# Performance work log

Measured on AMD Instinct MI355X. Metric: run time of the kernel, lower is better.

## Reference

```python
import jax, jax.numpy as jnp
import numpy as np

G1 = 3.0  # cfg.TRAIN.IoU_Gamma1
G2 = 1.0  # cfg.TRAIN.IoU_Gamma2


def setup_inputs() -> dict:
    key = jax.random.key(0)
    ks = jax.random.split(key, 5)
    B, N = 16, 2048
    cls = 0.3 * jax.random.normal(ks[0], (B, N, 2), jnp.float32)
    label_cls = jax.random.randint(ks[1], (B, N), 0, 2).astype(jnp.int32)
    label_loc = jax.random.normal(ks[2], (B, 4, N), jnp.float32)
    pred_bboxes = jax.random.uniform(ks[3], (B, 4, N), jnp.float32)
    label_target = jax.random.uniform(ks[4], (B, 4), jnp.float32)
    dataset_id = jnp.zeros((B,), jnp.int32)
    return dict(cls=cls, label_cls=label_cls, label_loc=label_loc,
                pred_bboxes=pred_bboxes, label_target=label_target,
                dataset_id=dataset_id)


def _iou(boxes, target):
    # boxes [B,4,N] (x1,y1,x2,y2); target [B,4]
    x1, y1, x2, y2 = boxes[:, 0], boxes[:, 1], boxes[:, 2], boxes[:, 3]
    tx1, ty1, tx2, ty2 = (target[:, 0:1], target[:, 1:2],
                          target[:, 2:3], target[:, 3:4])
    ww = jnp.clip(jnp.minimum(tx2, x2) - jnp.maximum(tx1, x1), 0.0)
    hh = jnp.clip(jnp.minimum(ty2, y2) - jnp.maximum(ty1, y1), 0.0)
    area = (x2 - x1) * (y2 - y1)
    ta = (tx2 - tx1) * (ty2 - ty1)
    inter = ww * hh
    return inter / (area + ta - inter)  # [B,N]


def _forward(cls, label_loc, pred_bboxes, label_target, label_cls, dataset_id):
    prob = jnp.exp(cls[..., 1])                      # [B,N]
    pos = label_cls > 0                              # [B,N]
    iou = _iou(pred_bboxes, label_target)            # [B,N]
    # centerness distance to target center
    cx = label_loc[:, 0] + label_target[:, 0:1]      # [B,N]
    cy = label_loc[:, 1] + label_target[:, 1:2]
    tcx = (label_target[:, 0] + label_target[:, 2]) * 0.5
    tcy = (label_target[:, 1] + label_target[:, 3]) * 0.5
    d = jnp.sqrt((cx - tcx[:, None]) ** 2 + (cy - tcy[:, None]) ** 2)  # [B,N]
    # pair (p,q): both positive, d[q]-d[p] >= 1.0 (== nested sorted-loop selection)
    pair = (pos[:, :, None] & pos[:, None, :]
            & ((d[:, None, :] - d[:, :, None]) >= 1.0))               # [B,N,N]
    m = pair.astype(prob.dtype)
    cnt = m.sum((1, 2))                                               # [B]
    # guard exponent with the mask to avoid inf*0 on dead pairs
    e1 = jnp.where(pair, -G1 * (prob[:, :, None] - prob[:, None, :]), 0.0)
    iou_sg = jax.lax.stop_gradient(iou)
    e2 = jnp.where(pair, -G2 * (iou[:, :, None] - iou_sg[:, None, :]), 0.0)
    denom = jnp.maximum(cnt, 1.0)
    l1 = (jnp.exp(e1) * m).sum((1, 2)) / denom                        # [B]
    l2 = (jnp.exp(e2) * m).sum((1, 2)) / denom
    valid = ((dataset_id != 1) & (cnt > 0)).astype(prob.dtype)        # [B]
    nv = valid.sum()
    safe_nv = jnp.maximum(nv, 1.0)
    f1 = jnp.where(nv > 0, (l1 * valid).sum() / safe_nv, 0.0)
    f2 = jnp.where(nv > 0, (l2 * valid).sum() / safe_nv, 0.0)
    return (f1, f2)


def reference(cls, label_cls, label_loc, pred_bboxes, label_target, dataset_id):
    return _forward(cls, label_loc, pred_bboxes, label_target, label_cls, dataset_id)
```

## Files before the change

### kernel.cpp

```cpp
#include <hip/hip_runtime.h>


#define G1 3.0f
#define G2 1.0f

constexpr int B    = 16;
constexpr int N    = 2048;
constexpr int TJ   = 64;
constexpr int IPT  = 8;
constexpr int JCH  = N / TJ;
constexpr int NBLK = B * JCH;

__device__ unsigned g_cnt;

__global__ void __launch_bounds__(256)
igr_kernel(const float* __restrict__ cls, const int* __restrict__ label_cls,
           const float* __restrict__ label_loc, const float* __restrict__ pred,
           const float* __restrict__ tgt, const int* __restrict__ dataset_id,
           double* __restrict__ part, float* __restrict__ out) {
  __shared__ uint4  stile[TJ];
  __shared__ float  ssd[TJ];
  __shared__ float  suf1[TJ + 1], suf2[TJ + 1];
  __shared__ double red[3][4];
  __shared__ double bl1[B], bl2[B], bval[B];
  __shared__ unsigned s_last;

  const int bid  = blockIdx.x;
  const int b    = bid >> 5;
  const int jc   = bid & 31;
  const int t    = threadIdx.x;
  const int base = b * N;

  const float tx1 = tgt[b * 4 + 0], ty1 = tgt[b * 4 + 1];
  const float tx2 = tgt[b * 4 + 2], ty2 = tgt[b * 4 + 3];
  const float ta  = (tx2 - tx1) * (ty2 - ty1);
  const float tcx = (tx1 + tx2) * 0.5f, tcy = (ty1 + ty2) * 0.5f;

  const float* __restrict__ pb = pred      + (size_t)b * 4 * N;
  const float* __restrict__ lb = label_loc + (size_t)b * 4 * N;

  auto elem = [&](int n, float& d, float& prob, float& iou, bool& pos) {
    float x1 = pb[n], y1 = pb[N + n], x2 = pb[2 * N + n], y2 = pb[3 * N + n];
    float ww = fmaxf(fminf(tx2, x2) - fmaxf(tx1, x1), 0.f);
    float hh = fmaxf(fminf(ty2, y2) - fmaxf(ty1, y1), 0.f);
    float inter = ww * hh;
    iou  = inter / ((x2 - x1) * (y2 - y1) + ta - inter);
    prob = __expf(cls[((size_t)(base + n)) * 2 + 1]);
    pos  = label_cls[base + n] > 0;
    float cx = lb[n] + tx1, cy = lb[N + n] + ty1;
    float dx = cx - tcx, dy = cy - tcy;
    d = sqrtf(dx * dx + dy * dy);
  };

  float dm_j = 0.f; unsigned uj = 0u;
  if (t < TJ) {
    float d, prob, iou; bool pos;
    elem(jc * TJ + t, d, prob, iou, pos);
    dm_j = pos ? d : -1e30f;
    uj = __float_as_uint(dm_j);
    uj ^= (uj & 0x80000000u) ? 0xFFFFFFFFu : 0x80000000u;
    stile[t] = make_uint4(uj, (unsigned)t,
                          __float_as_uint(__expf(G1 * prob)),
                          __float_as_uint(__expf(G2 * iou)));
  }
  if (t == TJ) { suf1[TJ] = 0.f; suf2[TJ] = 0.f; }

  float di[IPT], v1i[IPT], v2i[IPT];
#pragma unroll
  for (int k = 0; k < IPT; ++k) {
    float d, prob, iou; bool pos;
    elem(k * 256 + t, d, prob, iou, pos);
    di[k]  = d;
    v1i[k] = pos ? __expf(-G1 * prob) : 0.f;
    v2i[k] = pos ? __expf(-G2 * iou)  : 0.f;
  }
  __syncthreads();

  if (t < TJ) {
    const unsigned long long mykey = ((unsigned long long)uj << 32) | (unsigned)t;
    int rank = 0; float s1 = 0.f, s2 = 0.f;
#pragma unroll 8
    for (int q = 0; q < TJ; ++q) {
      uint4 v = stile[q];
      unsigned long long kq = ((unsigned long long)v.x << 32) | v.y;
      bool lt = kq < mykey;
      rank += lt ? 1 : 0;
      s1 += lt ? 0.f : __uint_as_float(v.z);
      s2 += lt ? 0.f : __uint_as_float(v.w);
    }
    ssd[rank] = dm_j; suf1[rank] = s1; suf2[rank] = s2;
  }
  __syncthreads();

  double p1 = 0.0, p2 = 0.0; int cnt = 0;
#pragma unroll
  for (int k = 0; k < IPT; ++k) {
    const float d = di[k];
    int kk = 0;
#pragma unroll
    for (int w = TJ >> 1; w > 0; w >>= 1)
      kk += (ssd[kk + w - 1] - d >= 1.0f) ? 0 : w;
    kk += (ssd[kk] - d >= 1.0f) ? 0 : 1;
    p1 += (double)v1i[k] * (double)suf1[kk];
    p2 += (double)v2i[k] * (double)suf2[kk];
    cnt += (v1i[k] > 0.f) ? (TJ - kk) : 0;
  }
  double pc = (double)cnt;

  for (int off = 32; off; off >>= 1) {
    p1 += __shfl_down(p1, off);
    p2 += __shfl_down(p2, off);
    pc += __shfl_down(pc, off);
  }
  const int wv = t >> 6, lane = t & 63;
  if (lane == 0) { red[0][wv] = p1; red[1][wv] = p2; red[2][wv] = pc; }
  __syncthreads();

  if (t == 0) {
    double a = red[0][0] + red[0][1] + red[0][2] + red[0][3];
    double c = red[1][0] + red[1][1] + red[1][2] + red[1][3];
    double e = red[2][0] + red[2][1] + red[2][2] + red[2][3];
    unsigned long long* pp = (unsigned long long*)(part + (size_t)bid * 3);
    unsigned long long o0 = atomicExch(pp + 0, __double_as_longlong(a));
    unsigned long long o1 = atomicExch(pp + 1, __double_as_longlong(c));
    unsigned long long o2 = atomicExch(pp + 2, __double_as_longlong(e));
    asm volatile("" :: "v"(o0), "v"(o1), "v"(o2));
    unsigned old = atomicAdd(&g_cnt, 1u);
    s_last = (old == (unsigned)(NBLK - 1)) ? 1u : 0u;
  }
  __syncthreads();

  if (s_last) {
    const int tb = t >> 4, kq = t & 15;
    double q1 = 0, q2 = 0, qc = 0;
#pragma unroll
    for (int h = 0; h < 2; ++h) {
      size_t p = (size_t)(tb * JCH + kq + h * 16) * 3;
      unsigned long long* pp = (unsigned long long*)part;
      q1 += __longlong_as_double(atomicOr(pp + p + 0, 0ull));
      q2 += __longlong_as_double(atomicOr(pp + p + 1, 0ull));
      qc += __longlong_as_double(atomicOr(pp + p + 2, 0ull));
    }
    for (int off = 8; off; off >>= 1) {
      q1 += __shfl_down(q1, off, 16);
      q2 += __shfl_down(q2, off, 16);
      qc += __shfl_down(qc, off, 16);
    }
    if (kq == 0) {
      bool valid = (dataset_id[tb] != 1) && (qc > 0.0);
      double denom = fmax(qc, 1.0);
      bl1[tb]  = valid ? q1 / denom : 0.0;
      bl2[tb]  = valid ? q2 / denom : 0.0;
      bval[tb] = valid ? 1.0 : 0.0;
    }
    __syncthreads();
    if (t == 0) {
      double nv = 0, f1 = 0, f2 = 0;
      for (int x = 0; x < B; ++x) { nv += bval[x]; f1 += bl1[x]; f2 += bl2[x]; }
      out[0] = (float)((nv > 0) ? f1 / nv : 0.0);
      out[1] = (float)((nv > 0) ? f2 / nv : 0.0);
      atomicExch(&g_cnt, 0u);
    }
  }
}

extern "C" void kernel_launch(void* const* d_in, const int* in_sizes, int n_in,
                              void* d_out, int out_size, void* d_ws, size_t ws_size,
                              hipStream_t stream) {
  const float* cls       = (const float*)d_in[0];
  const int*   label_cls = (const int*)d_in[1];
  const float* label_loc = (const float*)d_in[2];
  const float* pred      = (const float*)d_in[3];
  const float* tgt       = (const float*)d_in[4];
  const int*   dset      = (const int*)d_in[5];

  double* part = (double*)d_ws;

  igr_kernel<<<NBLK, 256, 0, stream>>>(cls, label_cls, label_loc, pred, tgt,
                                       dset, part, (float*)d_out);
}
```

Measured before the change: 20.77 us.

## Vectorize per-thread input loads and split completion reduction into per-batch stages

Each thread now loads four contiguous elements per field with float4/int4 loads instead of eight strided scalar loads. This cuts the number of memory instructions in the i-side prologue, and the order of the i elements does not matter for the pair sums. The single global last-block reduction is also replaced by a two-level scheme: the last block of each batch reduces its 32 partials, writes a per-batch result, and the last batch leader then combines the 16 batch results. This shortens the serial tail work done by one block, at the cost of extra global counters, a second atomic handshake and more workspace use.

```diff
diff --git a/kernel.cpp b/kernel.cpp
--- a/kernel.cpp
+++ b/kernel.cpp
@@ -11,19 +11,20 @@
 constexpr int JCH  = N / TJ;
 constexpr int NBLK = B * JCH;
 
-__device__ unsigned g_cnt;
+__device__ unsigned g_cnt_b[B];
+__device__ unsigned g_cnt_f;
 
 __global__ void __launch_bounds__(256)
 igr_kernel(const float* __restrict__ cls, const int* __restrict__ label_cls,
            const float* __restrict__ label_loc, const float* __restrict__ pred,
            const float* __restrict__ tgt, const int* __restrict__ dataset_id,
-           double* __restrict__ part, float* __restrict__ out) {
+           double* __restrict__ part, double* __restrict__ bres,
+           float* __restrict__ out) {
   __shared__ uint4  stile[TJ];
   __shared__ float  ssd[TJ];
   __shared__ float  suf1[TJ + 1], suf2[TJ + 1];
   __shared__ double red[3][4];
-  __shared__ double bl1[B], bl2[B], bval[B];
-  __shared__ unsigned s_last;
+  __shared__ unsigned s_lead, s_final;
 
   const int bid  = blockIdx.x;
   const int b    = bid >> 5;
@@ -39,23 +40,19 @@
   const float* __restrict__ pb = pred      + (size_t)b * 4 * N;
   const float* __restrict__ lb = label_loc + (size_t)b * 4 * N;
 
-  auto elem = [&](int n, float& d, float& prob, float& iou, bool& pos) {
+  float dm_j = 0.f; unsigned uj = 0u;
+  if (t < TJ) {
+    const int n = jc * TJ + t;
     float x1 = pb[n], y1 = pb[N + n], x2 = pb[2 * N + n], y2 = pb[3 * N + n];
     float ww = fmaxf(fminf(tx2, x2) - fmaxf(tx1, x1), 0.f);
     float hh = fmaxf(fminf(ty2, y2) - fmaxf(ty1, y1), 0.f);
     float inter = ww * hh;
-    iou  = inter / ((x2 - x1) * (y2 - y1) + ta - inter);
-    prob = __expf(cls[((size_t)(base + n)) * 2 + 1]);
-    pos  = label_cls[base + n] > 0;
+    float iou  = inter / ((x2 - x1) * (y2 - y1) + ta - inter);
+    float prob = __expf(cls[((size_t)(base + n)) * 2 + 1]);
+    bool  pos  = label_cls[base + n] > 0;
     float cx = lb[n] + tx1, cy = lb[N + n] + ty1;
     float dx = cx - tcx, dy = cy - tcy;
-    d = sqrtf(dx * dx + dy * dy);
-  };
-
-  float dm_j = 0.f; unsigned uj = 0u;
-  if (t < TJ) {
-    float d, prob, iou; bool pos;
-    elem(jc * TJ + t, d, prob, iou, pos);
+    float d  = sqrtf(dx * dx + dy * dy);
     dm_j = pos ? d : -1e30f;
     uj = __float_as_uint(dm_j);
     uj ^= (uj & 0x80000000u) ? 0xFFFFFFFFu : 0x80000000u;
@@ -65,14 +62,48 @@
   }
   if (t == TJ) { suf1[TJ] = 0.f; suf2[TJ] = 0.f; }
 
+  const float4* __restrict__ pb4 = (const float4*)pb;
+  const float4* __restrict__ lb4 = (const float4*)lb;
+  const float4* __restrict__ cl4 = (const float4*)(cls + (size_t)base * 2);
+  const int4*   __restrict__ lc4 = (const int4*)(label_cls + base);
+
   float di[IPT], v1i[IPT], v2i[IPT];
 #pragma unroll
-  for (int k = 0; k < IPT; ++k) {
-    float d, prob, iou; bool pos;
-    elem(k * 256 + t, d, prob, iou, pos);
-    di[k]  = d;
-    v1i[k] = pos ? __expf(-G1 * prob) : 0.f;
-    v2i[k] = pos ? __expf(-G2 * iou)  : 0.f;
+  for (int h = 0; h < 2; ++h) {
+    const int w = h * 256 + t;
+    const float4 X1 = pb4[0 * (N / 4) + w];
+    const float4 Y1 = pb4[1 * (N / 4) + w];
+    const float4 X2 = pb4[2 * (N / 4) + w];
+    const float4 Y2 = pb4[3 * (N / 4) + w];
+    const float4 CX = lb4[0 * (N / 4) + w];
+    const float4 CY = lb4[1 * (N / 4) + w];
+    const float4 C0 = cl4[2 * w + 0];
+    const float4 C1 = cl4[2 * w + 1];
+    const int4   LC = lc4[w];
+    const float x1v[4] = {X1.x, X1.y, X1.z, X1.w};
+    const float y1v[4] = {Y1.x, Y1.y, Y1.z, Y1.w};
+    const float x2v[4] = {X2.x, X2.y, X2.z, X2.w};
+    const float y2v[4] = {Y2.x, Y2.y, Y2.z, Y2.w};
+    const float cxv[4] = {CX.x, CX.y, CX.z, CX.w};
+    const float cyv[4] = {CY.x, CY.y, CY.z, CY.w};
+    const float clv[4] = {C0.y, C0.w, C1.y, C1.w};
+    const int   lcv[4] = {LC.x, LC.y, LC.z, LC.w};
+#pragma unroll
+    for (int c = 0; c < 4; ++c) {
+      const int k = h * 4 + c;
+      float x1 = x1v[c], y1 = y1v[c], x2 = x2v[c], y2 = y2v[c];
+      float ww = fmaxf(fminf(tx2, x2) - fmaxf(tx1, x1), 0.f);
+      float hh = fmaxf(fminf(ty2, y2) - fmaxf(ty1, y1), 0.f);
+      float inter = ww * hh;
+      float iou  = inter / ((x2 - x1) * (y2 - y1) + ta - inter);
+      float prob = __expf(clv[c]);
+      bool  pos  = lcv[c] > 0;
+      float cx = cxv[c] + tx1, cy = cyv[c] + ty1;
+      float dx = cx - tcx, dy = cy - tcy;
+      di[k]  = sqrtf(dx * dx + dy * dy);
+      v1i[k] = pos ? __expf(-G1 * prob) : 0.f;
+      v2i[k] = pos ? __expf(-G2 * iou)  : 0.f;
+    }
   }
   __syncthreads();
 
@@ -125,41 +156,60 @@
     unsigned long long o1 = atomicExch(pp + 1, __double_as_longlong(c));
     unsigned long long o2 = atomicExch(pp + 2, __double_as_longlong(e));
     asm volatile("" :: "v"(o0), "v"(o1), "v"(o2));
-    unsigned old = atomicAdd(&g_cnt, 1u);
-    s_last = (old == (unsigned)(NBLK - 1)) ? 1u : 0u;
-  }
-  __syncthreads();
-
-  if (s_last) {
-    const int tb = t >> 4, kq = t & 15;
+    unsigned old = atomicAdd(&g_cnt_b[b], 1u);
+    s_lead = (old == (unsigned)(JCH - 1)) ? 1u : 0u;
+  }
+  __syncthreads();
+
+  if (s_lead) {
     double q1 = 0, q2 = 0, qc = 0;
-#pragma unroll
-    for (int h = 0; h < 2; ++h) {
-      size_t p = (size_t)(tb * JCH + kq + h * 16) * 3;
-      unsigned long long* pp = (unsigned long long*)part;
-      q1 += __longlong_as_double(atomicOr(pp + p + 0, 0ull));
-      q2 += __longlong_as_double(atomicOr(pp + p + 1, 0ull));
-      qc += __longlong_as_double(atomicOr(pp + p + 2, 0ull));
-    }
-    for (int off = 8; off; off >>= 1) {
-      q1 += __shfl_down(q1, off, 16);
-      q2 += __shfl_down(q2, off, 16);
-      qc += __shfl_down(qc, off, 16);
-    }
-    if (kq == 0) {
-      bool valid = (dataset_id[tb] != 1) && (qc > 0.0);
+    if (t < JCH) {
+      unsigned long long* pp =
+          (unsigned long long*)(part + (size_t)(b * JCH + t) * 3);
+      q1 = __longlong_as_double(atomicOr(pp + 0, 0ull));
+      q2 = __longlong_as_double(atomicOr(pp + 1, 0ull));
+      qc = __longlong_as_double(atomicOr(pp + 2, 0ull));
+    }
+    for (int off = 16; off; off >>= 1) {
+      q1 += __shfl_down(q1, off);
+      q2 += __shfl_down(q2, off);
+      qc += __shfl_down(qc, off);
+    }
+    if (t == 0) {
+      bool valid = (dataset_id[b] != 1) && (qc > 0.0);
       double denom = fmax(qc, 1.0);
-      bl1[tb]  = valid ? q1 / denom : 0.0;
-      bl2[tb]  = valid ? q2 / denom : 0.0;
-      bval[tb] = valid ? 1.0 : 0.0;
+      double l1 = valid ? q1 / denom : 0.0;
+      double l2 = valid ? q2 / denom : 0.0;
+      double vv = valid ? 1.0 : 0.0;
+      unsigned long long* rp = (unsigned long long*)(bres + (size_t)b * 3);
+      unsigned long long r0 = atomicExch(rp + 0, __double_as_longlong(l1));
+      unsigned long long r1 = atomicExch(rp + 1, __double_as_longlong(l2));
+      unsigned long long r2 = atomicExch(rp + 2, __double_as_longlong(vv));
+      asm volatile("" :: "v"(r0), "v"(r1), "v"(r2));
+      unsigned old2 = atomicAdd(&g_cnt_f, 1u);
+      s_final = (old2 == (unsigned)(B - 1)) ? 1u : 0u;
     }
     __syncthreads();
-    if (t == 0) {
-      double nv = 0, f1 = 0, f2 = 0;
-      for (int x = 0; x < B; ++x) { nv += bval[x]; f1 += bl1[x]; f2 += bl2[x]; }
-      out[0] = (float)((nv > 0) ? f1 / nv : 0.0);
-      out[1] = (float)((nv > 0) ? f2 / nv : 0.0);
-      atomicExch(&g_cnt, 0u);
+
+    if (s_final) {
+      double r1 = 0, r2 = 0, rv = 0;
+      if (t < B) {
+        unsigned long long* rp = (unsigned long long*)(bres + (size_t)t * 3);
+        r1 = __longlong_as_double(atomicOr(rp + 0, 0ull));
+        r2 = __longlong_as_double(atomicOr(rp + 1, 0ull));
+        rv = __longlong_as_double(atomicOr(rp + 2, 0ull));
+      }
+      for (int off = 8; off; off >>= 1) {
+        r1 += __shfl_down(r1, off);
+        r2 += __shfl_down(r2, off);
+        rv += __shfl_down(rv, off);
+      }
+      if (t == 0) {
+        out[0] = (float)((rv > 0) ? r1 / rv : 0.0);
+        out[1] = (float)((rv > 0) ? r2 / rv : 0.0);
+        atomicExch(&g_cnt_f, 0u);
+      }
+      if (t < B) atomicExch(&g_cnt_b[t], 0u);
     }
   }
 }
@@ -175,7 +225,8 @@
   const int*   dset      = (const int*)d_in[5];
 
   double* part = (double*)d_ws;
+  double* bres = part + (size_t)NBLK * 3;
 
   igr_kernel<<<NBLK, 256, 0, stream>>>(cls, label_cls, label_loc, pred, tgt,
-                                       dset, part, (float*)d_out);
+                                       dset, part, bres, (float*)d_out);
 }
```

Result: slower. 23.01 us (+10.8%).
